# Kernel optimization log

Hardware: AMD Instinct MI355X
Metric: run time of the kernel (lower is better)

Reference implementation:

```python
import jax, jax.numpy as jnp
import numpy as np

N_QUBITS = 12
DEPTH = 4
OUT_DIM = 2
HID = 64
BATCH = 4096


def _u3(a, b, c):
    """Combined RZ(c) @ RY(b) @ RX(a) single-qubit gate, batched. a,b,c: [B] -> [B,2,2] complex."""
    ca, sa = jnp.cos(a / 2), jnp.sin(a / 2)
    cb, sb = jnp.cos(b / 2), jnp.sin(b / 2)
    RX = jnp.stack([jnp.stack([ca + 0j, -1j * sa], -1),
                    jnp.stack([-1j * sa, ca + 0j], -1)], -2)
    RY = jnp.stack([jnp.stack([cb + 0j, -sb + 0j], -1),
                    jnp.stack([sb + 0j, cb + 0j], -1)], -2)
    ez = jnp.exp(-1j * c / 2)
    zeros = jnp.zeros_like(ez)
    RZ = jnp.stack([jnp.stack([ez, zeros], -1),
                    jnp.stack([zeros, jnp.conj(ez)], -1)], -2)
    return jnp.einsum('bij,bjk,bkl->bil', RZ, RY, RX)


def _apply_1q(psi, U, q):
    """psi: [B]+[2]*n (wire 0 = most significant), U: [B,2,2]."""
    psi = jnp.moveaxis(psi, q + 1, 1)
    shp = psi.shape
    psi = psi.reshape(shp[0], 2, -1)
    psi = jnp.einsum('bij,bjr->bir', U, psi)
    return jnp.moveaxis(psi.reshape(shp), 1, q + 1)


def _apply_cnot(psi, c, t):
    """CNOT with control c, target t on psi [B]+[2]*n."""
    s0 = jax.lax.index_in_dim(psi, 0, axis=c + 1, keepdims=True)
    s1 = jax.lax.index_in_dim(psi, 1, axis=c + 1, keepdims=True)
    s1 = jnp.flip(s1, axis=t + 1)
    return jnp.concatenate([s0, s1], axis=c + 1)


def _circuit_expvals(params):
    """Batched hardware-efficient ansatz state-vector sim.
    params: [B, DEPTH, N_QUBITS, 3] -> PauliZ expvals [B, N_QUBITS]."""
    B = params.shape[0]
    n = N_QUBITS
    psi = jnp.zeros((B, 2 ** n), jnp.complex64).at[:, 0].set(1.0)
    psi = psi.reshape((B,) + (2,) * n)
    for l in range(DEPTH):
        for q in range(n):  # RX, RY, RZ per qubit (fused to one 2x2)
            U = _u3(params[:, l, q, 0], params[:, l, q, 1], params[:, l, q, 2])
            psi = _apply_1q(psi, U, q)
        for q in range(n):   # ring of CNOTs
            psi = _apply_cnot(psi, q, (q + 1) % n)
    probs = (psi.real ** 2 + psi.imag ** 2).reshape(B, 2 ** n)
    idx = jnp.arange(2 ** n)
    bits = (idx[None, :] >> (n - 1 - jnp.arange(n))[:, None]) & 1  # [n, 2^n]
    signs = (1.0 - 2.0 * bits).astype(jnp.float32)
    return probs @ signs.T  # <Z_q> = p(bit=0) - p(bit=1)


def setup_inputs() -> dict:
    key = jax.random.key(0)
    ks = jax.random.split(key, 5)
    n = N_QUBITS
    n_params = DEPTH * n * 3
    def w(k, shape):
        return (jax.random.normal(k, shape, jnp.float32) / np.sqrt(shape[0])).astype(jnp.float32)
    return {
        'noise': jax.random.normal(ks[0], (BATCH, n), jnp.float32),
        'W1': w(ks[1], (n, HID)), 'b1': jnp.zeros((HID,), jnp.float32),
        'W2': w(ks[2], (HID, n_params)), 'b2': jnp.zeros((n_params,), jnp.float32),
        'W3': w(ks[3], (n, HID)), 'b3': jnp.zeros((HID,), jnp.float32),
        'W4': w(ks[4], (HID, OUT_DIM)), 'b4': jnp.zeros((OUT_DIM,), jnp.float32),
    }


def reference(noise, W1, b1, W2, b2, W3, b3, W4, b4):
    h = jnp.tanh(noise @ W1 + b1)
    circ_params = (h @ W2 + b2).reshape(noise.shape[0], DEPTH, N_QUBITS, 3)
    meas = _circuit_expvals(circ_params)          # [B, n_qubits]
    h2 = jnp.tanh(meas @ W3 + b3)
    return h2 @ W4 + b4                            # [B, output_dim]
```

## Files before the change

kernel.cpp:

```cpp
#include <hip/hip_runtime.h>
#include <math.h>

#define NQ  12
#define TPB 256


struct GF12 { unsigned row[12]; };

constexpr GF12 gf_id(){ GF12 m{}; for(int i=0;i<12;i++) m.row[i]=1u<<i; return m; }
constexpr GF12 gf_mul(const GF12&A,const GF12&B){
  GF12 r{};
  for(int i=0;i<12;i++){ unsigned acc=0;
    for(int k=0;k<12;k++) if((A.row[i]>>k)&1u) acc ^= B.row[k];
    r.row[i]=acc; }
  return r;
}
constexpr GF12 gf_cnot(int q){ GF12 m=gf_id(); int c=11-q, t=11-((q+1)%12); m.row[t]^=(1u<<c); return m; }

struct Red { unsigned arr[12]; int hb[12]; int n; };
constexpr unsigned red_reduce(const Red& R, unsigned y){
  for(int i=0;i<R.n;i++) if((y>>R.hb[i])&1u) y ^= R.arr[i];
  return y;
}
constexpr bool red_add(Red& R, unsigned cand){
  unsigned y = red_reduce(R, cand);
  if(!y) return false;
  int h=0;
  for(int b2=11;b2>=1;b2--) if((y>>b2)&1u){ h=b2; break; }
  R.arr[R.n]=y; R.hb[R.n]=h; R.n++;
  return true;
}

struct Tab4 {
  unsigned B[12][8];
  unsigned C[12][16];
  unsigned M[12][4];
  unsigned mq[12];
  unsigned uq[12];
  bool ok;
};

constexpr Tab4 make4(){
  Tab4 T{}; T.ok=true;
  GF12 D=gf_id(); for(int q=0;q<12;q++) D=gf_mul(gf_cnot(q),D);
  GF12 Cm=gf_id(); for(int q=11;q>=0;q--) Cm=gf_mul(gf_cnot(q),Cm);
  unsigned V[12][4]{},R[12][4]{},rfin[12]{};
  GF12 Mm=gf_id(), Mi=gf_id();
  for(int l=0;l<4;l++){
    for(int q=0;q<12;q++){
      int b=11-q; unsigned v=0;
      for(int j=0;j<12;j++) v|=((Mi.row[j]>>b)&1u)<<j;
      V[l*3+q/4][q&3]=v; R[l*3+q/4][q&3]=Mm.row[b];
    }
    Mm=gf_mul(D,Mm); Mi=gf_mul(Cm,Mi);
  }
  for(int q=0;q<12;q++) rfin[q]=Mm.row[11-q];

  for(int p=0;p<12;p++){
    for(int j=0;j<4;j++) for(int i=0;i<4;i++){
      int par=__builtin_popcount(R[p][j]&V[p][i])&1;
      if(par!=((i==j)?1:0)) T.ok=false;
    }
    Red S{};
    for(int i=0;i<4;i++) if(!red_add(S,V[p][i])) T.ok=false;
    for(int k=0;k<4;k++){
      unsigned pick=0;
      for(unsigned m=0;m<256 && !pick;m++){
        unsigned x=(1u<<k)|(m<<4);
        if(red_reduce(S,x)) pick=x;
      }
      if(!pick){ T.ok=false; pick=1u<<k; }
      red_add(S,pick); T.B[p][k]=pick;
    }
    for(int k=4;k<6;k++){
      unsigned pick=0;
      for(unsigned m=1;m<256 && !pick;m++){
        unsigned x=m<<4;
        if(red_reduce(S,x)) pick=x;
      }
      if(!pick){ T.ok=false; pick=16; }
      red_add(S,pick); T.B[p][k]=pick;
    }
    for(int k=6;k<8;k++){
      unsigned pick=0;
      for(unsigned x=1;x<4096 && !pick;x++){
        if(red_reduce(S,x)) pick=x;
      }
      if(!pick){ T.ok=false; pick=1; }
      red_add(S,pick); T.B[p][k]=pick;
    }
    if(S.n!=12) T.ok=false;
    for(int z=0;z<16;z++){
      unsigned c=0;
      for(int i=0;i<4;i++) if((z>>i)&1) c^=V[p][i];
      T.C[p][z]=c;
    }
    for(int j=0;j<4;j++){
      unsigned m=0;
      for(int i=0;i<8;i++) m|=(unsigned)(__builtin_popcount(R[p][j]&T.B[p][i])&1)<<i;
      T.M[p][j]=m;
    }
  }
  for(int q=0;q<12;q++){
    unsigned u=0,m=0;
    for(int i=0;i<4;i++) u|=(unsigned)(__builtin_popcount(rfin[q]&V[11][i])&1)<<i;
    for(int i=0;i<8;i++) m|=(unsigned)(__builtin_popcount(rfin[q]&T.B[11][i])&1)<<i;
    T.uq[q]=u; T.mq[q]=m;
  }
  return T;
}

constexpr Tab4 hT4 = make4();
static_assert(hT4.ok, "GF(2) in-place table self-check failed");
__constant__ Tab4 cT4 = hT4;

#define SR(n_) (((n_)&1) ? Q[(n_)>>1].z : Q[(n_)>>1].x)
#define SI(n_) (((n_)&1) ? Q[(n_)>>1].w : Q[(n_)>>1].y)

#define GATE(MM,JJ) do { \
    const int _lb = pl + 4*(JJ); \
    const unsigned _sg = ((unsigned)(__popc((MM) & (unsigned)t) & 1)) << 31; \
    const float ar = __uint_as_float((unsigned)__builtin_amdgcn_readlane((int)cur, _lb+0)); \
    const float ai = __uint_as_float(((unsigned)__builtin_amdgcn_readlane((int)cur, _lb+1)) ^ _sg); \
    const float br = __uint_as_float(((unsigned)__builtin_amdgcn_readlane((int)cur, _lb+2)) ^ _sg); \
    const float bi = __uint_as_float((unsigned)__builtin_amdgcn_readlane((int)cur, _lb+3)); \
    _Pragma("unroll") \
    for (int s0=0; s0<16; ++s0){ \
      if ((s0 >> (JJ)) & 1) continue; \
      const int s1 = s0 | (1<<(JJ)); \
      const float xr=SR(s0), xi=SI(s0), yr=SR(s1), yi=SI(s1); \
      SR(s0)=fmaf(ar,xr,fmaf(-ai,xi,fmaf(br,yr,-(bi*yi)))); \
      SI(s0)=fmaf(ar,xi,fmaf( ai,xr,fmaf(br,yi,  bi*yr ))); \
      SR(s1)=fmaf(ar,yr,fmaf( ai,yi,fmaf(-br,xr,-(bi*xi)))); \
      SI(s1)=fmaf(ar,yi,fmaf(-ai,yr,fmaf( bi,xr,-(br*xi)))); \
    } \
  } while(0)

__global__ void __launch_bounds__(TPB, 5)
qgen(const float* __restrict__ noise,
     const float* __restrict__ W1, const float* __restrict__ b1,
     const float* __restrict__ W2, const float* __restrict__ b2,
     const float* __restrict__ W3, const float* __restrict__ b3,
     const float* __restrict__ W4, const float* __restrict__ b4,
     float* __restrict__ out)
{
  __shared__ float2 s2[4096];
  float*  sf = (float*)s2;
  float4* s4 = (float4*)s2;

  const int t = threadIdx.x;
  const int b = blockIdx.x;
  const int lane = t & 63;

  if (t < 12) sf[400+t] = noise[b*12+t];
  __syncthreads();
  if (t < 64){
    float a = b1[t];
    #pragma unroll
    for (int k=0;k<12;++k) a = fmaf(sf[400+k], W1[k*64+t], a);
    sf[192+t] = tanhf(a);
  }
  __syncthreads();
  if (t < 144){
    float a = b2[t];
    #pragma unroll 16
    for (int j=0;j<64;++j) a = fmaf(sf[192+j], W2[j*144+t], a);
    sf[256+t] = a;
  }
  __syncthreads();
  if (t < 48){
    float aa = sf[256+3*t+0]*0.5f, bb = sf[256+3*t+1]*0.5f, c = sf[256+3*t+2]*0.5f;
    float sa,ca,sb,cb,sc2,cc;
    __sincosf(aa,&sa,&ca); __sincosf(bb,&sb,&cb); __sincosf(c,&sc2,&cc);
    float A=cb*ca, B=sb*sa, Cc=sb*ca, Dd=cb*sa;
    s4[t] = make_float4(fmaf(cc,A,  sc2*B),  fmaf(cc,B, -sc2*A),
                        fmaf(-cc,Cc,-sc2*Dd), fmaf(sc2,Cc,-cc*Dd));
  }
  __syncthreads();
  const unsigned* su = (const unsigned*)s2;
  const unsigned cu0 = su[lane], cu1 = su[64+lane], cu2 = su[128+lane];
  __syncthreads();

  float4 Q[8];
  unsigned addr[16];

  {
    #pragma unroll
    for (int k=0;k<8;++k) Q[k] = make_float4(0.f,0.f,0.f,0.f);
    if (t==0) Q[0].x = 1.0f;
    const unsigned cur = cu0; const int pl = 0;
    GATE(cT4.M[0][0],0); GATE(cT4.M[0][1],1); GATE(cT4.M[0][2],2); GATE(cT4.M[0][3],3);
    unsigned rep = 0;
    #pragma unroll
    for (int i=0;i<8;++i) rep ^= (((unsigned)t>>i)&1u) ? cT4.B[0][i] : 0u;
    #pragma unroll
    for (int z=0;z<16;++z) s2[rep ^ cT4.C[0][z]] = make_float2(SR(z), SI(z));
  }
  __syncthreads();

  #pragma unroll 1
  for (int p=1; p<12; ++p){
    unsigned rep = 0;
    #pragma unroll
    for (int i=0;i<8;++i) rep ^= (((unsigned)t>>i)&1u) ? cT4.B[p][i] : 0u;
    #pragma unroll
    for (int z=0;z<16;++z) addr[z] = rep ^ cT4.C[p][z];
    #pragma unroll
    for (int z=0;z<16;++z){ float2 v2 = s2[addr[z]]; SR(z)=v2.x; SI(z)=v2.y; }

    const int ps = p>>2;
    const unsigned cur = (ps==0)?cu0:((ps==1)?cu1:cu2);
    const int pl = (p&3)<<4;
    GATE(cT4.M[p][0],0); GATE(cT4.M[p][1],1); GATE(cT4.M[p][2],2); GATE(cT4.M[p][3],3);

    if (p < 11){
      #pragma unroll
      for (int z=0;z<16;++z) s2[addr[z]] = make_float2(SR(z), SI(z));
      __syncthreads();
    }
  }

  float H[16];
  #pragma unroll
  for (int z=0;z<16;++z) H[z] = fmaf(SR(z),SR(z), SI(z)*SI(z));
  #pragma unroll
  for (int st=1; st<16; st<<=1){
    #pragma unroll
    for (int z=0;z<16;++z){
      if (z & st) continue;
      float a0=H[z], a1=H[z|st];
      H[z]=a0+a1; H[z|st]=a0-a1;
    }
  }
  float acc[12];
  #pragma unroll
  for (int q=0;q<12;++q){
    const unsigned ls = ((unsigned)(__popc(cT4.mq[q] & (unsigned)t) & 1)) << 31;
    acc[q] = __uint_as_float(__float_as_uint(H[cT4.uq[q]]) ^ ls);
  }

  __syncthreads();
  const int wv = t >> 6;
  #pragma unroll
  for (int q=0;q<12;++q){
    float v = acc[q];
    #pragma unroll
    for (int off=32; off>0; off>>=1) v += __shfl_down(v, off, 64);
    if (lane==0) sf[wv*12+q] = v;
  }
  __syncthreads();
  if (t < 12) sf[64+t] = sf[t] + sf[12+t] + sf[24+t] + sf[36+t];
  __syncthreads();

  if (t < 64){
    float a = b3[t];
    #pragma unroll
    for (int k=0;k<12;++k) a = fmaf(sf[64+k], W3[k*64+t], a);
    float h2 = tanhf(a);
    float p0 = h2*W4[2*t+0], p1 = h2*W4[2*t+1];
    #pragma unroll
    for (int off=32; off>0; off>>=1){ p0 += __shfl_down(p0,off,64); p1 += __shfl_down(p1,off,64); }
    if (t==0){ out[2*b+0]=p0+b4[0]; out[2*b+1]=p1+b4[1]; }
  }
}

extern "C" void kernel_launch(void* const* d_in, const int* in_sizes, int n_in,
                              void* d_out, int out_size, void* d_ws, size_t ws_size,
                              hipStream_t stream)
{
  const float* noise = (const float*)d_in[0];
  const float* W1 = (const float*)d_in[1];
  const float* b1 = (const float*)d_in[2];
  const float* W2 = (const float*)d_in[3];
  const float* b2 = (const float*)d_in[4];
  const float* W3 = (const float*)d_in[5];
  const float* b3 = (const float*)d_in[6];
  const float* W4 = (const float*)d_in[7];
  const float* b4 = (const float*)d_in[8];
  float* out = (float*)d_out;
  const int batch = in_sizes[0] / NQ;
  qgen<<<batch, TPB, 0, stream>>>(noise, W1, b1, W2, b2, W3, b3, W4, b4, out);
}
```

Measured before the change: 237.3 us.

## Pair gate passes so each shared-memory block barrier covers two passes

Rebuilds the GF(2) basis tables so that consecutive pass pairs (p0,p1) share a common 10-dimensional subspace and the same two high basis vectors. Each thread then reads and writes the same set of shared-memory locations in both passes of a pair, so the barrier after the even pass can be dropped. This halves the number of __syncthreads per circuit simulation. It adds constexpr table construction complexity and relies on the compile-time self-checks to guarantee there are no cross-thread hazards.

```diff
diff --git a/kernel.cpp b/kernel.cpp
--- a/kernel.cpp
+++ b/kernel.cpp
@@ -56,62 +56,99 @@
   }
   for(int q=0;q<12;q++) rfin[q]=Mm.row[11-q];
 
-  for(int p=0;p<12;p++){
-    for(int j=0;j<4;j++) for(int i=0;i<4;i++){
-      int par=__builtin_popcount(R[p][j]&V[p][i])&1;
-      if(par!=((i==j)?1:0)) T.ok=false;
-    }
+  for(int m=0;m<6;m++){
+    const int p0=2*m, p1=p0+1;
     Red S{};
-    for(int i=0;i<4;i++) if(!red_add(S,V[p][i])) T.ok=false;
-    for(int k=0;k<4;k++){
-      unsigned pick=0;
-      for(unsigned m=0;m<256 && !pick;m++){
-        unsigned x=(1u<<k)|(m<<4);
-        if(red_reduce(S,x)) pick=x;
-      }
-      if(!pick){ T.ok=false; pick=1u<<k; }
-      red_add(S,pick); T.B[p][k]=pick;
-    }
-    for(int k=4;k<6;k++){
-      unsigned pick=0;
-      for(unsigned m=1;m<256 && !pick;m++){
-        unsigned x=m<<4;
-        if(red_reduce(S,x)) pick=x;
-      }
-      if(!pick){ T.ok=false; pick=16; }
-      red_add(S,pick); T.B[p][k]=pick;
-    }
-    for(int k=6;k<8;k++){
-      unsigned pick=0;
-      for(unsigned x=1;x<4096 && !pick;x++){
-        if(red_reduce(S,x)) pick=x;
-      }
-      if(!pick){ T.ok=false; pick=1; }
-      red_add(S,pick); T.B[p][k]=pick;
-    }
-    if(S.n!=12) T.ok=false;
-    for(int z=0;z<16;z++){
-      unsigned c=0;
-      for(int i=0;i<4;i++) if((z>>i)&1) c^=V[p][i];
-      T.C[p][z]=c;
-    }
-    for(int j=0;j<4;j++){
-      unsigned m=0;
-      for(int i=0;i<8;i++) m|=(unsigned)(__builtin_popcount(R[p][j]&T.B[p][i])&1)<<i;
-      T.M[p][j]=m;
+    for(int i=0;i<4;i++){ red_add(S,V[p0][i]); red_add(S,V[p1][i]); }
+    for(unsigned x=1; x<4096 && S.n<10; x++) red_add(S,x);
+    if(S.n!=10) T.ok=false;
+    unsigned W6=0,W7=0;
+    { Red SB=S;
+      for(unsigned x=1;x<4096 && !W6;x++) if(red_reduce(SB,x)){ W6=x; red_add(SB,x); }
+      for(unsigned x=1;x<4096 && !W7;x++) if(red_reduce(SB,x)){ W7=x; red_add(SB,x); }
+      if(!W6||!W7) T.ok=false;
+    }
+    for(int pi=0; pi<2; pi++){
+      const int p = (pi==0)?p0:p1;
+      for(int j=0;j<4;j++) for(int i=0;i<4;i++){
+        int par=__builtin_popcount(R[p][j]&V[p][i])&1;
+        if(par!=((i==j)?1:0)) T.ok=false;
+      }
+      Red P{};
+      for(int i=0;i<4;i++) if(!red_add(P,V[p][i])) T.ok=false;
+      for(int k=0;k<4;k++){
+        unsigned pick=0;
+        for(unsigned hi=0;hi<256 && !pick;hi++){
+          unsigned x=(1u<<k)|(hi<<4);
+          if(red_reduce(S,x)) continue;
+          if(!red_reduce(P,x)) continue;
+          pick=x;
+        }
+        if(!pick){
+          for(unsigned x=1;x<4096 && !pick;x++){
+            if(red_reduce(S,x)) continue;
+            if(!red_reduce(P,x)) continue;
+            pick=x;
+          }
+        }
+        if(!pick){ T.ok=false; pick=1u<<k; }
+        red_add(P,pick); T.B[p][k]=pick;
+      }
+      for(int k=4;k<6;k++){
+        unsigned pick=0;
+        for(unsigned hi=1;hi<256 && !pick;hi++){
+          unsigned x=hi<<4;
+          if(red_reduce(S,x)) continue;
+          if(!red_reduce(P,x)) continue;
+          pick=x;
+        }
+        if(!pick){
+          for(unsigned x=1;x<4096 && !pick;x++){
+            if(red_reduce(S,x)) continue;
+            if(!red_reduce(P,x)) continue;
+            pick=x;
+          }
+        }
+        if(!pick){ T.ok=false; pick=16; }
+        red_add(P,pick); T.B[p][k]=pick;
+      }
+      T.B[p][6]=W6; T.B[p][7]=W7;
+      if(P.n!=10) T.ok=false;
+      { Red F=P;
+        if(!red_add(F,W6)) T.ok=false;
+        if(!red_add(F,W7)) T.ok=false;
+        if(F.n!=12) T.ok=false; }
+      for(int z=0;z<16;z++){
+        unsigned c=0;
+        for(int i=0;i<4;i++) if((z>>i)&1) c^=V[p][i];
+        T.C[p][z]=c;
+      }
+      for(int j=0;j<4;j++){
+        unsigned mm=0;
+        for(int i=0;i<8;i++) mm|=(unsigned)(__builtin_popcount(R[p][j]&T.B[p][i])&1)<<i;
+        T.M[p][j]=mm;
+      }
+    }
+    { Red S0{};
+      for(int i=0;i<4;i++) red_add(S0,V[p0][i]);
+      for(int i=0;i<6;i++) red_add(S0,T.B[p0][i]);
+      if(S0.n!=10) T.ok=false;
+      for(int i=0;i<6;i++) if(red_reduce(S0,T.B[p1][i])) T.ok=false;
+      for(int i=0;i<4;i++) if(red_reduce(S0,V[p1][i])) T.ok=false;
+      if(T.B[p0][6]!=T.B[p1][6] || T.B[p0][7]!=T.B[p1][7]) T.ok=false;
     }
   }
   for(int q=0;q<12;q++){
-    unsigned u=0,m=0;
+    unsigned u=0,mm=0;
     for(int i=0;i<4;i++) u|=(unsigned)(__builtin_popcount(rfin[q]&V[11][i])&1)<<i;
-    for(int i=0;i<8;i++) m|=(unsigned)(__builtin_popcount(rfin[q]&T.B[11][i])&1)<<i;
-    T.uq[q]=u; T.mq[q]=m;
+    for(int i=0;i<8;i++) mm|=(unsigned)(__builtin_popcount(rfin[q]&T.B[11][i])&1)<<i;
+    T.uq[q]=u; T.mq[q]=mm;
   }
   return T;
 }
 
 constexpr Tab4 hT4 = make4();
-static_assert(hT4.ok, "GF(2) in-place table self-check failed");
+static_assert(hT4.ok, "GF(2) paired in-place table self-check failed");
 __constant__ Tab4 cT4 = hT4;
 
 #define SR(n_) (((n_)&1) ? Q[(n_)>>1].z : Q[(n_)>>1].x)
@@ -196,7 +233,6 @@
     #pragma unroll
     for (int z=0;z<16;++z) s2[rep ^ cT4.C[0][z]] = make_float2(SR(z), SI(z));
   }
-  __syncthreads();
 
   #pragma unroll 1
   for (int p=1; p<12; ++p){
@@ -216,7 +252,7 @@
     if (p < 11){
       #pragma unroll
       for (int z=0;z<16;++z) s2[addr[z]] = make_float2(SR(z), SI(z));
-      __syncthreads();
+      if (p & 1) __syncthreads();
     }
   }
 
```

After: 240.6 us. About the same (+1.4%).

## Pair qubit groups and exchange amplitudes via intra-wave bpermute instead of LDS

Applied to the files above, without the earlier changes.

Reorganises the 12 gate passes into 6 pairs. Within a pair, the second group's amplitudes are redistributed across lanes with ds_bpermute, and the basis is chosen so the exchange stays inside a wavefront. LDS round-trips and block barriers therefore drop from 11 to 5, and the LDS writes become swizzled contiguous float4 stores. All address and permutation tables become compile-time constants. This aims to cut LDS traffic and sync cost, but adds 32 bpermutes per pair and a second register array, which raises register pressure.

```diff
diff --git a/kernel.cpp b/kernel.cpp
--- a/kernel.cpp
+++ b/kernel.cpp
@@ -15,7 +15,26 @@
     r.row[i]=acc; }
   return r;
 }
+constexpr unsigned gf_apply(const GF12&A, unsigned x){
+  unsigned y=0;
+  for(int i=0;i<12;i++) y |= (unsigned)(__builtin_popcount(A.row[i]&x)&1)<<i;
+  return y;
+}
 constexpr GF12 gf_cnot(int q){ GF12 m=gf_id(); int c=11-q, t=11-((q+1)%12); m.row[t]^=(1u<<c); return m; }
+constexpr GF12 gf_inv(const GF12&A){
+  unsigned a[12], inv[12];
+  for(int i=0;i<12;i++){ a[i]=A.row[i]; inv[i]=1u<<i; }
+  for(int c=0;c<12;c++){
+    int p=-1;
+    for(int r2=c;r2<12;r2++) if((a[r2]>>c)&1u){p=r2;break;}
+    if(p<0) continue;
+    unsigned ta=a[c]; a[c]=a[p]; a[p]=ta;
+    unsigned ti=inv[c]; inv[c]=inv[p]; inv[p]=ti;
+    for(int r2=0;r2<12;r2++) if(r2!=c && ((a[r2]>>c)&1u)){ a[r2]^=a[c]; inv[r2]^=inv[c]; }
+  }
+  GF12 R{}; for(int i=0;i<12;i++) R.row[i]=inv[i];
+  return R;
+}
 
 struct Red { unsigned arr[12]; int hb[12]; int n; };
 constexpr unsigned red_reduce(const Red& R, unsigned y){
@@ -31,17 +50,15 @@
   return true;
 }
 
-struct Tab4 {
-  unsigned B[12][8];
-  unsigned C[12][16];
-  unsigned M[12][4];
-  unsigned mq[12];
-  unsigned uq[12];
-  bool ok;
+struct PairT {
+  unsigned M0[4], M1[4];
+  unsigned sz[16], gx[16];
+  unsigned rB[8], roff[16];
 };
-
-constexpr Tab4 make4(){
-  Tab4 T{}; T.ok=true;
+struct AllT { PairT pr[6]; unsigned mq[12], uq[12]; bool ok; };
+
+constexpr AllT makeAll(){
+  AllT T{}; T.ok=true;
   GF12 D=gf_id(); for(int q=0;q<12;q++) D=gf_mul(gf_cnot(q),D);
   GF12 Cm=gf_id(); for(int q=11;q>=0;q--) Cm=gf_mul(gf_cnot(q),Cm);
   unsigned V[12][4]{},R[12][4]{},rfin[12]{};
@@ -56,68 +73,142 @@
   }
   for(int q=0;q<12;q++) rfin[q]=Mm.row[11-q];
 
-  for(int p=0;p<12;p++){
-    for(int j=0;j<4;j++) for(int i=0;i<4;i++){
-      int par=__builtin_popcount(R[p][j]&V[p][i])&1;
+  GF12 Sg=gf_id(); Sg.row[1]|=1u<<4; Sg.row[2]|=1u<<5; Sg.row[3]|=1u<<6;
+
+  GF12 Tprev{}, Tprev_inv{};
+  for(int m=0;m<6;m++){
+    const int p0=2*m, p1=p0+1;
+    for(int pp=p0;pp<=p1;pp++) for(int j=0;j<4;j++) for(int i=0;i<4;i++){
+      int par=__builtin_popcount(R[pp][j]&V[pp][i])&1;
       if(par!=((i==j)?1:0)) T.ok=false;
     }
     Red S{};
-    for(int i=0;i<4;i++) if(!red_add(S,V[p][i])) T.ok=false;
-    for(int k=0;k<4;k++){
+    for(int i=0;i<4;i++){ red_add(S,V[p0][i]); red_add(S,V[p1][i]); }
+    for(unsigned x=1;x<4096 && S.n<10;x++) red_add(S,x);
+    if(S.n!=10) T.ok=false;
+    Red S12=S, RA{}, RB{};
+    for(int i=0;i<4;i++){ red_add(RA,V[p0][i]); red_add(RB,V[p1][i]); }
+    unsigned B[8]{};
+    Red resR{};
+    for(int k=0;k<6;k++){
       unsigned pick=0;
-      for(unsigned m=0;m<256 && !pick;m++){
-        unsigned x=(1u<<k)|(m<<4);
-        if(red_reduce(S,x)) pick=x;
-      }
-      if(!pick){ T.ok=false; pick=1u<<k; }
-      red_add(S,pick); T.B[p][k]=pick;
-    }
-    for(int k=4;k<6;k++){
-      unsigned pick=0;
-      for(unsigned m=1;m<256 && !pick;m++){
-        unsigned x=m<<4;
-        if(red_reduce(S,x)) pick=x;
-      }
-      if(!pick){ T.ok=false; pick=16; }
-      red_add(S,pick); T.B[p][k]=pick;
+      if(m>0){
+        unsigned res=(k<4)?(1u<<k):0u;
+        for(unsigned hi=(k<4)?0u:1u; hi<256 && !pick; hi++){
+          unsigned y=res|(hi<<4);
+          unsigned x=gf_apply(Tprev_inv,y);
+          if(red_reduce(S,x)) continue;
+          if(!red_reduce(RA,x)) continue;
+          if(!red_reduce(RB,x)) continue;
+          pick=x;
+        }
+        for(unsigned y=1;y<4096 && !pick;y++){
+          unsigned x=gf_apply(Tprev_inv,y);
+          if(red_reduce(S,x)) continue;
+          if(!red_reduce(RA,x)) continue;
+          if(!red_reduce(RB,x)) continue;
+          if(k<4){ unsigned rb=y&15u; if(!rb || !red_reduce(resR,rb)) continue; }
+          pick=x;
+        }
+      }
+      if(!pick){
+        for(unsigned x=1;x<4096 && !pick;x++){
+          if(red_reduce(S,x)) continue;
+          if(!red_reduce(RA,x)) continue;
+          if(!red_reduce(RB,x)) continue;
+          pick=x;
+        }
+      }
+      if(!pick){ T.ok=false; pick=1; }
+      if(m>0 && k<4){ unsigned rb=gf_apply(Tprev,pick)&15u; if(rb) red_add(resR,rb); }
+      red_add(RA,pick); red_add(RB,pick);
+      B[k]=pick;
     }
     for(int k=6;k<8;k++){
       unsigned pick=0;
-      for(unsigned x=1;x<4096 && !pick;x++){
-        if(red_reduce(S,x)) pick=x;
-      }
+      for(unsigned x=1;x<4096 && !pick;x++) if(red_reduce(S12,x)) pick=x;
       if(!pick){ T.ok=false; pick=1; }
-      red_add(S,pick); T.B[p][k]=pick;
-    }
-    if(S.n!=12) T.ok=false;
+      red_add(S12,pick); B[k]=pick;
+    }
+    if(S12.n!=12) T.ok=false;
+    GF12 Z{};
+    for(int i=0;i<12;i++){
+      unsigned rr=0;
+      for(int k=0;k<4;k++) rr |= ((V[p1][k]>>i)&1u)<<k;
+      for(int k=0;k<8;k++) rr |= ((B[k]>>i)&1u)<<(4+k);
+      Z.row[i]=rr;
+    }
+    GF12 Tp=gf_inv(Z);
+    { GF12 I2=gf_mul(Tp,Z); for(int i=0;i<12;i++) if(I2.row[i]!=(1u<<i)) T.ok=false; }
+    for(int j=0;j<4;j++){
+      unsigned m0=0,m1=0;
+      for(int k=0;k<8;k++){
+        m0 |= (unsigned)(__builtin_popcount(R[p0][j]&B[k])&1)<<k;
+        m1 |= (unsigned)(__builtin_popcount(R[p1][j]&B[k])&1)<<k;
+      }
+      T.pr[m].M0[j]=m0; T.pr[m].M1[j]=m1;
+    }
+    unsigned zeta[4]{}, gam[4]{};
+    for(int i=0;i<4;i++){
+      unsigned d=gf_apply(Tp,V[p0][i]);
+      if(d>>10) T.ok=false;
+      zeta[i]=d&15u; gam[i]=(d>>4)&63u;
+    }
+    unsigned zmap[16]{}; bool seen[16]{};
     for(int z=0;z<16;z++){
-      unsigned c=0;
-      for(int i=0;i<4;i++) if((z>>i)&1) c^=V[p][i];
-      T.C[p][z]=c;
-    }
-    for(int j=0;j<4;j++){
-      unsigned m=0;
-      for(int i=0;i<8;i++) m|=(unsigned)(__builtin_popcount(R[p][j]&T.B[p][i])&1)<<i;
-      T.M[p][j]=m;
-    }
-  }
-  for(int q=0;q<12;q++){
-    unsigned u=0,m=0;
-    for(int i=0;i<4;i++) u|=(unsigned)(__builtin_popcount(rfin[q]&V[11][i])&1)<<i;
-    for(int i=0;i<8;i++) m|=(unsigned)(__builtin_popcount(rfin[q]&T.B[11][i])&1)<<i;
-    T.uq[q]=u; T.mq[q]=m;
+      unsigned zz=0;
+      for(int i=0;i<4;i++) if((z>>i)&1) zz^=zeta[i];
+      zmap[z]=zz;
+      if(seen[zz]) T.ok=false; seen[zz]=true;
+    }
+    for(int zp=0;zp<16;zp++){
+      unsigned src=0;
+      for(int z=0;z<16;z++) if(zmap[z]==(unsigned)zp) src=(unsigned)z;
+      unsigned gg=0;
+      for(int i=0;i<4;i++) if((src>>i)&1) gg^=gam[i];
+      T.pr[m].sz[zp]=src; T.pr[m].gx[zp]=gg;
+    }
+    for(int z=0;z<16;z++){
+      unsigned c0=0,c1=0,gg=0,bb=0;
+      for(int i=0;i<4;i++){
+        if((z>>i)&1){ c0^=V[p0][i]; gg^=gam[i]; }
+        if((zmap[z]>>i)&1) c1^=V[p1][i];
+      }
+      for(int k=0;k<6;k++) if((gg>>k)&1) bb^=B[k];
+      if((c0^c1^bb)!=0) T.ok=false;
+    }
+    if(m>0){
+      for(int k=0;k<8;k++) T.pr[m].rB[k]=gf_apply(Tprev,B[k]);
+      for(int z=0;z<16;z++){
+        unsigned c=0;
+        for(int i=0;i<4;i++) if((z>>i)&1) c^=V[p0][i];
+        T.pr[m].roff[z]=gf_apply(Tprev,c);
+      }
+    }
+    GF12 Tnew=gf_mul(Sg,Tp), Tnew_inv=gf_mul(Z,Sg);
+    { GF12 I2=gf_mul(Tnew,Tnew_inv); for(int i=0;i<12;i++) if(I2.row[i]!=(1u<<i)) T.ok=false; }
+    Tprev=Tnew; Tprev_inv=Tnew_inv;
+    if(m==5){
+      for(int q=0;q<12;q++){
+        unsigned u=0,mm=0;
+        for(int i=0;i<4;i++) u |= (unsigned)(__builtin_popcount(rfin[q]&V[11][i])&1)<<i;
+        for(int k=0;k<8;k++) mm |= (unsigned)(__builtin_popcount(rfin[q]&B[k])&1)<<k;
+        T.uq[q]=u; T.mq[q]=mm;
+      }
+    }
   }
   return T;
 }
 
-constexpr Tab4 hT4 = make4();
-static_assert(hT4.ok, "GF(2) in-place table self-check failed");
-__constant__ Tab4 cT4 = hT4;
+constexpr AllT hA = makeAll();
+static_assert(hA.ok, "GF(2) paired-bpermute table self-check failed");
 
 #define SR(n_) (((n_)&1) ? Q[(n_)>>1].z : Q[(n_)>>1].x)
 #define SI(n_) (((n_)&1) ? Q[(n_)>>1].w : Q[(n_)>>1].y)
-
-#define GATE(MM,JJ) do { \
+#define NR(n_) (((n_)&1) ? Qn[(n_)>>1].z : Qn[(n_)>>1].x)
+#define NI(n_) (((n_)&1) ? Qn[(n_)>>1].w : Qn[(n_)>>1].y)
+
+#define GATE_BODY(RD,ID,MM,JJ) do { \
     const int _lb = pl + 4*(JJ); \
     const unsigned _sg = ((unsigned)(__popc((MM) & (unsigned)t) & 1)) << 31; \
     const float ar = __uint_as_float((unsigned)__builtin_amdgcn_readlane((int)cur, _lb+0)); \
@@ -128,13 +219,52 @@
     for (int s0=0; s0<16; ++s0){ \
       if ((s0 >> (JJ)) & 1) continue; \
       const int s1 = s0 | (1<<(JJ)); \
-      const float xr=SR(s0), xi=SI(s0), yr=SR(s1), yi=SI(s1); \
-      SR(s0)=fmaf(ar,xr,fmaf(-ai,xi,fmaf(br,yr,-(bi*yi)))); \
-      SI(s0)=fmaf(ar,xi,fmaf( ai,xr,fmaf(br,yi,  bi*yr ))); \
-      SR(s1)=fmaf(ar,yr,fmaf( ai,yi,fmaf(-br,xr,-(bi*xi)))); \
-      SI(s1)=fmaf(ar,yi,fmaf(-ai,yr,fmaf( bi,xr,-(br*xi)))); \
+      const float xr=RD(s0), xi=ID(s0), yr=RD(s1), yi=ID(s1); \
+      RD(s0)=fmaf(ar,xr,fmaf(-ai,xi,fmaf(br,yr,-(bi*yi)))); \
+      ID(s0)=fmaf(ar,xi,fmaf( ai,xr,fmaf(br,yi,  bi*yr ))); \
+      RD(s1)=fmaf(ar,yr,fmaf( ai,yi,fmaf(-br,xr,-(bi*xi)))); \
+      ID(s1)=fmaf(ar,yi,fmaf(-ai,yr,fmaf( bi,xr,-(br*xi)))); \
     } \
   } while(0)
+#define GATEQ(MM,JJ) GATE_BODY(SR,SI,MM,JJ)
+#define GATEN(MM,JJ) GATE_BODY(NR,NI,MM,JJ)
+
+template<int M>
+__device__ __forceinline__ void do_pair(float4 Q[8], float4 Qn[8],
+                                        unsigned c0, unsigned c1, unsigned c2,
+                                        unsigned t, float2* s2, float4* s4)
+{
+  constexpr PairT P = hA.pr[M];
+  if constexpr (M > 0){
+    unsigned base=0;
+    #pragma unroll
+    for(int k=0;k<8;++k) base ^= ((t>>k)&1u) ? P.rB[k] : 0u;
+    #pragma unroll
+    for(int z=0;z<16;++z){ float2 v=s2[base ^ P.roff[z]]; SR(z)=v.x; SI(z)=v.y; }
+  }
+  { constexpr int ci=(2*M)>>2;
+    const unsigned cur=(ci==0)?c0:((ci==1)?c1:c2);
+    const int pl=((2*M)&3)<<4;
+    GATEQ(P.M0[0],0); GATEQ(P.M0[1],1); GATEQ(P.M0[2],2); GATEQ(P.M0[3],3); }
+  { const unsigned t4=t<<2;
+    #pragma unroll
+    for(int zp=0; zp<16; ++zp){
+      const int idx=(int)(t4 ^ (P.gx[zp]<<2));
+      NR(zp)=__uint_as_float((unsigned)__builtin_amdgcn_ds_bpermute(idx,(int)__float_as_uint(SR(P.sz[zp]))));
+      NI(zp)=__uint_as_float((unsigned)__builtin_amdgcn_ds_bpermute(idx,(int)__float_as_uint(SI(P.sz[zp]))));
+    } }
+  { constexpr int ci=(2*M+1)>>2;
+    const unsigned cur=(ci==0)?c0:((ci==1)?c1:c2);
+    const int pl=((2*M+1)&3)<<4;
+    GATEN(P.M1[0],0); GATEN(P.M1[1],1); GATEN(P.M1[2],2); GATEN(P.M1[3],3); }
+  if constexpr (M < 5){
+    __syncthreads();
+    const unsigned wb=t<<3;
+    #pragma unroll
+    for(int k=0;k<8;++k) s4[wb | ((unsigned)k ^ (t&7u))] = Qn[k];
+    __syncthreads();
+  }
+}
 
 __global__ void __launch_bounds__(TPB, 5)
 qgen(const float* __restrict__ noise,
@@ -145,10 +275,10 @@
      float* __restrict__ out)
 {
   __shared__ float2 s2[4096];
-  float*  sf = (float*)s2;
-  float4* s4 = (float4*)s2;
-
-  const int t = threadIdx.x;
+  float*  sf=(float*)s2;
+  float4* s4=(float4*)s2;
+
+  const unsigned t = threadIdx.x;
   const int b = blockIdx.x;
   const int lane = t & 63;
 
@@ -177,90 +307,64 @@
                         fmaf(-cc,Cc,-sc2*Dd), fmaf(sc2,Cc,-cc*Dd));
   }
   __syncthreads();
-  const unsigned* su = (const unsigned*)s2;
-  const unsigned cu0 = su[lane], cu1 = su[64+lane], cu2 = su[128+lane];
-  __syncthreads();
-
-  float4 Q[8];
-  unsigned addr[16];
-
-  {
-    #pragma unroll
-    for (int k=0;k<8;++k) Q[k] = make_float4(0.f,0.f,0.f,0.f);
-    if (t==0) Q[0].x = 1.0f;
-    const unsigned cur = cu0; const int pl = 0;
-    GATE(cT4.M[0][0],0); GATE(cT4.M[0][1],1); GATE(cT4.M[0][2],2); GATE(cT4.M[0][3],3);
-    unsigned rep = 0;
-    #pragma unroll
-    for (int i=0;i<8;++i) rep ^= (((unsigned)t>>i)&1u) ? cT4.B[0][i] : 0u;
-    #pragma unroll
-    for (int z=0;z<16;++z) s2[rep ^ cT4.C[0][z]] = make_float2(SR(z), SI(z));
-  }
-  __syncthreads();
-
-  #pragma unroll 1
-  for (int p=1; p<12; ++p){
-    unsigned rep = 0;
-    #pragma unroll
-    for (int i=0;i<8;++i) rep ^= (((unsigned)t>>i)&1u) ? cT4.B[p][i] : 0u;
-    #pragma unroll
-    for (int z=0;z<16;++z) addr[z] = rep ^ cT4.C[p][z];
-    #pragma unroll
-    for (int z=0;z<16;++z){ float2 v2 = s2[addr[z]]; SR(z)=v2.x; SI(z)=v2.y; }
-
-    const int ps = p>>2;
-    const unsigned cur = (ps==0)?cu0:((ps==1)?cu1:cu2);
-    const int pl = (p&3)<<4;
-    GATE(cT4.M[p][0],0); GATE(cT4.M[p][1],1); GATE(cT4.M[p][2],2); GATE(cT4.M[p][3],3);
-
-    if (p < 11){
-      #pragma unroll
-      for (int z=0;z<16;++z) s2[addr[z]] = make_float2(SR(z), SI(z));
-      __syncthreads();
-    }
-  }
+  const unsigned* su=(const unsigned*)s2;
+  const unsigned cu0=su[lane], cu1=su[64+lane], cu2=su[128+lane];
+  __syncthreads();
+
+  float4 Q[8], Qn[8];
+  #pragma unroll
+  for(int k=0;k<8;++k) Q[k]=make_float4(0.f,0.f,0.f,0.f);
+  if(t==0) Q[0].x=1.0f;
+
+  do_pair<0>(Q,Qn,cu0,cu1,cu2,t,s2,s4);
+  do_pair<1>(Q,Qn,cu0,cu1,cu2,t,s2,s4);
+  do_pair<2>(Q,Qn,cu0,cu1,cu2,t,s2,s4);
+  do_pair<3>(Q,Qn,cu0,cu1,cu2,t,s2,s4);
+  do_pair<4>(Q,Qn,cu0,cu1,cu2,t,s2,s4);
+  do_pair<5>(Q,Qn,cu0,cu1,cu2,t,s2,s4);
 
   float H[16];
   #pragma unroll
-  for (int z=0;z<16;++z) H[z] = fmaf(SR(z),SR(z), SI(z)*SI(z));
-  #pragma unroll
-  for (int st=1; st<16; st<<=1){
-    #pragma unroll
-    for (int z=0;z<16;++z){
-      if (z & st) continue;
+  for(int z=0;z<16;++z) H[z]=fmaf(NR(z),NR(z), NI(z)*NI(z));
+  #pragma unroll
+  for(int st=1;st<16;st<<=1){
+    #pragma unroll
+    for(int z=0;z<16;++z){
+      if(z & st) continue;
       float a0=H[z], a1=H[z|st];
       H[z]=a0+a1; H[z|st]=a0-a1;
     }
   }
   float acc[12];
   #pragma unroll
-  for (int q=0;q<12;++q){
-    const unsigned ls = ((unsigned)(__popc(cT4.mq[q] & (unsigned)t) & 1)) << 31;
-    acc[q] = __uint_as_float(__float_as_uint(H[cT4.uq[q]]) ^ ls);
-  }
-
-  __syncthreads();
-  const int wv = t >> 6;
-  #pragma unroll
-  for (int q=0;q<12;++q){
-    float v = acc[q];
-    #pragma unroll
-    for (int off=32; off>0; off>>=1) v += __shfl_down(v, off, 64);
-    if (lane==0) sf[wv*12+q] = v;
-  }
-  __syncthreads();
-  if (t < 12) sf[64+t] = sf[t] + sf[12+t] + sf[24+t] + sf[36+t];
-  __syncthreads();
-
-  if (t < 64){
-    float a = b3[t];
-    #pragma unroll
-    for (int k=0;k<12;++k) a = fmaf(sf[64+k], W3[k*64+t], a);
-    float h2 = tanhf(a);
-    float p0 = h2*W4[2*t+0], p1 = h2*W4[2*t+1];
-    #pragma unroll
-    for (int off=32; off>0; off>>=1){ p0 += __shfl_down(p0,off,64); p1 += __shfl_down(p1,off,64); }
-    if (t==0){ out[2*b+0]=p0+b4[0]; out[2*b+1]=p1+b4[1]; }
+  for(int q=0;q<12;++q){
+    constexpr_pragma_dummy: ;
+    const unsigned ls=((unsigned)(__popc(hA.mq[q]&t)&1))<<31;
+    acc[q]=__uint_as_float(__float_as_uint(H[hA.uq[q]])^ls);
+  }
+
+  __syncthreads();
+  const int wv=t>>6;
+  #pragma unroll
+  for(int q=0;q<12;++q){
+    float v=acc[q];
+    #pragma unroll
+    for(int off=32;off>0;off>>=1) v += __shfl_down(v,off,64);
+    if(lane==0) sf[wv*12+q]=v;
+  }
+  __syncthreads();
+  if(t<12) sf[64+t]=sf[t]+sf[12+t]+sf[24+t]+sf[36+t];
+  __syncthreads();
+
+  if(t<64){
+    float a=b3[t];
+    #pragma unroll
+    for(int k=0;k<12;++k) a=fmaf(sf[64+k],W3[k*64+t],a);
+    float h2=tanhf(a);
+    float p0=h2*W4[2*t+0], p1=h2*W4[2*t+1];
+    #pragma unroll
+    for(int off=32;off>0;off>>=1){ p0+=__shfl_down(p0,off,64); p1+=__shfl_down(p1,off,64); }
+    if(t==0){ out[2*b+0]=p0+b4[0]; out[2*b+1]=p1+b4[1]; }
   }
 }
 
@@ -268,16 +372,16 @@
                               void* d_out, int out_size, void* d_ws, size_t ws_size,
                               hipStream_t stream)
 {
-  const float* noise = (const float*)d_in[0];
-  const float* W1 = (const float*)d_in[1];
-  const float* b1 = (const float*)d_in[2];
-  const float* W2 = (const float*)d_in[3];
-  const float* b2 = (const float*)d_in[4];
-  const float* W3 = (const float*)d_in[5];
-  const float* b3 = (const float*)d_in[6];
-  const float* W4 = (const float*)d_in[7];
-  const float* b4 = (const float*)d_in[8];
-  float* out = (float*)d_out;
-  const int batch = in_sizes[0] / NQ;
-  qgen<<<batch, TPB, 0, stream>>>(noise, W1, b1, W2, b2, W3, b3, W4, b4, out);
-}
+  const float* noise=(const float*)d_in[0];
+  const float* W1=(const float*)d_in[1];
+  const float* b1=(const float*)d_in[2];
+  const float* W2=(const float*)d_in[3];
+  const float* b2=(const float*)d_in[4];
+  const float* W3=(const float*)d_in[5];
+  const float* b3=(const float*)d_in[6];
+  const float* W4=(const float*)d_in[7];
+  const float* b4=(const float*)d_in[8];
+  float* out=(float*)d_out;
+  const int batch=in_sizes[0]/NQ;
+  qgen<<<batch,TPB,0,stream>>>(noise,W1,b1,W2,b2,W3,b3,W4,b4,out);
+}
```

Result: no change. 236.7 us (-0.2%).
